# Kernel optimization log

Measured on AMD Instinct MI355X. Metric: run time of the kernel, lower is better.

Reference implementation:

```python
import jax, jax.numpy as jnp
import numpy as np

N_NODES = 100000
N_EDGES = 3200000


def setup_inputs() -> dict:
    key = jax.random.key(0)
    k = jax.random.split(key, 6)
    x = jax.random.normal(k[0], (N_NODES, 3), dtype=jnp.float32)
    edge_index = jax.random.randint(k[1], (2, N_EDGES), 0, N_NODES, dtype=jnp.int64)
    # Glorot-ish init for the two GCNConv layers (3->16, 16->7), bias=True (PyG default)
    W1 = jax.random.normal(k[2], (3, 16), dtype=jnp.float32) * (1.0 / np.sqrt(3.0))
    b1 = jnp.zeros((16,), dtype=jnp.float32)
    W2 = jax.random.normal(k[3], (16, 7), dtype=jnp.float32) * (1.0 / np.sqrt(16.0))
    b2 = jnp.zeros((7,), dtype=jnp.float32)
    return {"x": x, "edge_index": edge_index, "W1": W1, "b1": b1, "W2": W2, "b2": b2}


def _gcn_conv(x, W, b, src, dst, norm, n_nodes):
    # x: [N, Fin]; src/dst/norm: [E+N] (self-loops appended); out: [N, Fout]
    h = x @ W                                   # small GEMM
    msg = h[src] * norm[:, None]                # gather + scale per edge
    out = jax.ops.segment_sum(msg, dst, num_segments=n_nodes)  # scatter-add
    return out + b


def reference(x, edge_index, W1, b1, W2, b2):
    n = x.shape[0]
    loop = jnp.arange(n, dtype=edge_index.dtype)
    src = jnp.concatenate([edge_index[0], loop])
    dst = jnp.concatenate([edge_index[1], loop])
    # symmetric normalization D^-1/2 (A+I) D^-1/2, deg counted at targets
    deg = jax.ops.segment_sum(jnp.ones(src.shape[0], dtype=x.dtype), dst, num_segments=n)
    dinv = jnp.where(deg > 0, jax.lax.rsqrt(deg), 0.0)
    norm = dinv[src] * dinv[dst]                # [E+N]

    h = _gcn_conv(x, W1, b1, src, dst, norm, n)
    h = jax.nn.relu(h)
    h = _gcn_conv(h, W2, b2, src, dst, norm, n)
    return jax.nn.log_softmax(h, axis=1)
```

## Files before the change

kernel.cpp:

```cpp
#include <hip/hip_runtime.h>
#include <hip/hip_fp16.h>
#include <math.h>

#define N_NODES 100000
#define N_EDGES 3200000
#define NB 512
#define NPB 196
#define CAP 7168
#define EPB 12544
#define NBLK ((N_EDGES + EPB - 1) / EPB)

#define FSCALE 1048576.0f
#define INV_FSCALE (1.0f / 1048576.0f)


__device__ inline float2 h2f2(unsigned int u) {
    __half2 h = *reinterpret_cast<__half2*>(&u);
    return make_float2(__low2float(h), __high2float(h));
}

__device__ inline int fx(float v) { return __float2int_rn(v * FSCALE); }

__global__ void k_zero(int* __restrict__ gcur) {
    int i = blockIdx.x * blockDim.x + threadIdx.x;
    if (i < NB) gcur[i] = 0;
}

__global__ void __launch_bounds__(1024) k_bucket(
        const int* __restrict__ ei, int* __restrict__ gcur,
        unsigned int* __restrict__ bdata) {
    __shared__ int cnt[NB];
    __shared__ int gb[NB];
    int blk = blockIdx.x, tid = threadIdx.x;
    int e0 = blk * EPB;
    int ecnt = min(EPB, N_EDGES - e0);
    const int* dst = ei + N_EDGES + e0;
    const int* src = ei + e0;

    if (tid < NB) cnt[tid] = 0;
    __syncthreads();
    for (int i = tid; i < ecnt; i += 4096) {
        int i1 = i + 1024, i2 = i + 2048, i3 = i + 3072;
        int d0 = dst[i];
        int d1 = (i1 < ecnt) ? dst[i1] : 0;
        int d2 = (i2 < ecnt) ? dst[i2] : 0;
        int d3 = (i3 < ecnt) ? dst[i3] : 0;
        atomicAdd(&cnt[d0 / NPB], 1);
        if (i1 < ecnt) atomicAdd(&cnt[d1 / NPB], 1);
        if (i2 < ecnt) atomicAdd(&cnt[d2 / NPB], 1);
        if (i3 < ecnt) atomicAdd(&cnt[d3 / NPB], 1);
    }
    __syncthreads();
    if (tid < NB) {
        int c = cnt[tid];
        gb[tid] = (c > 0) ? atomicAdd(&gcur[tid], c) : 0;
        cnt[tid] = 0;
    }
    __syncthreads();
    for (int i = tid; i < ecnt; i += 4096) {
        int i1 = i + 1024, i2 = i + 2048, i3 = i + 3072;
        int d0 = dst[i];
        int s0 = src[i];
        int d1 = (i1 < ecnt) ? dst[i1] : 0;
        int s1 = (i1 < ecnt) ? src[i1] : 0;
        int d2 = (i2 < ecnt) ? dst[i2] : 0;
        int s2 = (i2 < ecnt) ? src[i2] : 0;
        int d3 = (i3 < ecnt) ? dst[i3] : 0;
        int s3 = (i3 < ecnt) ? src[i3] : 0;
        {
            int b = d0 / NPB, dl = d0 - b * NPB;
            int pos = atomicAdd(&cnt[b], 1) + gb[b];
            if (pos < CAP) bdata[(size_t)b * CAP + pos] = ((unsigned)dl << 17) | (unsigned)s0;
        }
        if (i1 < ecnt) {
            int b = d1 / NPB, dl = d1 - b * NPB;
            int pos = atomicAdd(&cnt[b], 1) + gb[b];
            if (pos < CAP) bdata[(size_t)b * CAP + pos] = ((unsigned)dl << 17) | (unsigned)s1;
        }
        if (i2 < ecnt) {
            int b = d2 / NPB, dl = d2 - b * NPB;
            int pos = atomicAdd(&cnt[b], 1) + gb[b];
            if (pos < CAP) bdata[(size_t)b * CAP + pos] = ((unsigned)dl << 17) | (unsigned)s2;
        }
        if (i3 < ecnt) {
            int b = d3 / NPB, dl = d3 - b * NPB;
            int pos = atomicAdd(&cnt[b], 1) + gb[b];
            if (pos < CAP) bdata[(size_t)b * CAP + pos] = ((unsigned)dl << 17) | (unsigned)s3;
        }
    }
}

__global__ void k_deg(const int* __restrict__ gcur, const unsigned int* __restrict__ bdata,
                      const float* __restrict__ x, __half2* __restrict__ xh) {
    __shared__ int cnt[NPB];
    int b = blockIdx.x, t = threadIdx.x;
    for (int j = t; j < NPB; j += 512) cnt[j] = 0;
    __syncthreads();
    int n = min(gcur[b], CAP);
    const unsigned int* p = bdata + (size_t)b * CAP;
    for (int e = t; e < n; e += 512) atomicAdd(&cnt[p[e] >> 17], 1);
    __syncthreads();
    int base = b * NPB;
    for (int j = t; j < NPB; j += 512) {
        int i = base + j;
        if (i < N_NODES) {
            float di = rsqrtf((float)cnt[j] + 1.0f);
            xh[2 * i + 0] = __floats2half2_rn(di * x[3 * i + 0], di * x[3 * i + 1]);
            xh[2 * i + 1] = __floats2half2_rn(di * x[3 * i + 2], di);
        }
    }
}

__global__ void __launch_bounds__(1024) k_l1(
        const int* __restrict__ gcur, const unsigned int* __restrict__ bdata,
        const __half2* __restrict__ xh, const float* __restrict__ W1,
        const float* __restrict__ b1, const float* __restrict__ W2,
        uint4* __restrict__ th) {
    __shared__ int a[NPB * 3];
    int b = blockIdx.x, tid = threadIdx.x;
    for (int j = tid; j < NPB * 3; j += 1024) a[j] = 0;
    __syncthreads();
    int n = min(gcur[b], CAP);
    const unsigned int* p = bdata + (size_t)b * CAP;
    const uint2* xg = (const uint2*)xh;
    for (int e = tid; e < n; e += 4096) {
        int e1 = e + 1024, e2 = e + 2048, e3 = e + 3072;
        unsigned int pk0 = p[e];
        unsigned int pk1 = (e1 < n) ? p[e1] : 0u;
        unsigned int pk2 = (e2 < n) ? p[e2] : 0u;
        unsigned int pk3 = (e3 < n) ? p[e3] : 0u;
        uint2 g0 = xg[pk0 & 0x1FFFF];
        uint2 g1 = (e1 < n) ? xg[pk1 & 0x1FFFF] : make_uint2(0u, 0u);
        uint2 g2 = (e2 < n) ? xg[pk2 & 0x1FFFF] : make_uint2(0u, 0u);
        uint2 g3 = (e3 < n) ? xg[pk3 & 0x1FFFF] : make_uint2(0u, 0u);
        {
            int dl = pk0 >> 17;
            float2 f01 = h2f2(g0.x), f2w = h2f2(g0.y);
            atomicAdd(&a[dl * 3 + 0], fx(f01.x));
            atomicAdd(&a[dl * 3 + 1], fx(f01.y));
            atomicAdd(&a[dl * 3 + 2], fx(f2w.x));
        }
        if (e1 < n) {
            int dl = pk1 >> 17;
            float2 f01 = h2f2(g1.x), f2w = h2f2(g1.y);
            atomicAdd(&a[dl * 3 + 0], fx(f01.x));
            atomicAdd(&a[dl * 3 + 1], fx(f01.y));
            atomicAdd(&a[dl * 3 + 2], fx(f2w.x));
        }
        if (e2 < n) {
            int dl = pk2 >> 17;
            float2 f01 = h2f2(g2.x), f2w = h2f2(g2.y);
            atomicAdd(&a[dl * 3 + 0], fx(f01.x));
            atomicAdd(&a[dl * 3 + 1], fx(f01.y));
            atomicAdd(&a[dl * 3 + 2], fx(f2w.x));
        }
        if (e3 < n) {
            int dl = pk3 >> 17;
            float2 f01 = h2f2(g3.x), f2w = h2f2(g3.y);
            atomicAdd(&a[dl * 3 + 0], fx(f01.x));
            atomicAdd(&a[dl * 3 + 1], fx(f01.y));
            atomicAdd(&a[dl * 3 + 2], fx(f2w.x));
        }
    }
    __syncthreads();
    int base = b * NPB;
    for (int j = tid; j < NPB; j += 1024) {
        int i = base + j;
        if (i >= N_NODES) continue;
        uint2 gi = xg[i];
        float2 f01 = h2f2(gi.x);
        float2 f2w = h2f2(gi.y);
        float di = f2w.y;
        float a0 = di * ((float)a[j * 3 + 0] * INV_FSCALE + f01.x);
        float a1 = di * ((float)a[j * 3 + 1] * INV_FSCALE + f01.y);
        float a2 = di * ((float)a[j * 3 + 2] * INV_FSCALE + f2w.x);
        float r[16];
#pragma unroll
        for (int k = 0; k < 16; ++k)
            r[k] = fmaxf(a0 * W1[k] + a1 * W1[16 + k] + a2 * W1[32 + k] + b1[k], 0.0f);
        float t[7];
#pragma unroll
        for (int c = 0; c < 7; ++c) {
            float v = 0.0f;
#pragma unroll
            for (int k = 0; k < 16; ++k) v += r[k] * W2[7 * k + c];
            t[c] = di * v;
        }
        __half2 h0 = __floats2half2_rn(t[0], t[1]);
        __half2 h1 = __floats2half2_rn(t[2], t[3]);
        __half2 h2 = __floats2half2_rn(t[4], t[5]);
        __half2 h3 = __floats2half2_rn(t[6], di);
        uint4 pk;
        pk.x = *reinterpret_cast<unsigned int*>(&h0);
        pk.y = *reinterpret_cast<unsigned int*>(&h1);
        pk.z = *reinterpret_cast<unsigned int*>(&h2);
        pk.w = *reinterpret_cast<unsigned int*>(&h3);
        th[i] = pk;
    }
}

__global__ void __launch_bounds__(1024) k_l2(
        const int* __restrict__ gcur, const unsigned int* __restrict__ bdata,
        const uint4* __restrict__ th, const float* __restrict__ b2,
        float* __restrict__ out) {
    __shared__ int a[NPB * 7];
    int b = blockIdx.x, tid = threadIdx.x;
    for (int j = tid; j < NPB * 7; j += 1024) a[j] = 0;
    __syncthreads();
    int n = min(gcur[b], CAP);
    const unsigned int* p = bdata + (size_t)b * CAP;
    for (int e = tid; e < n; e += 4096) {
        int e1 = e + 1024, e2 = e + 2048, e3 = e + 3072;
        unsigned int pk0 = p[e];
        unsigned int pk1 = (e1 < n) ? p[e1] : 0u;
        unsigned int pk2 = (e2 < n) ? p[e2] : 0u;
        unsigned int pk3 = (e3 < n) ? p[e3] : 0u;
        uint4 g0 = th[pk0 & 0x1FFFF];
        uint4 g1 = (e1 < n) ? th[pk1 & 0x1FFFF] : make_uint4(0u, 0u, 0u, 0u);
        uint4 g2 = (e2 < n) ? th[pk2 & 0x1FFFF] : make_uint4(0u, 0u, 0u, 0u);
        uint4 g3 = (e3 < n) ? th[pk3 & 0x1FFFF] : make_uint4(0u, 0u, 0u, 0u);
        {
            int dl = pk0 >> 17;
            float2 u0 = h2f2(g0.x), u1 = h2f2(g0.y), u2 = h2f2(g0.z), u3 = h2f2(g0.w);
            atomicAdd(&a[dl * 7 + 0], fx(u0.x));
            atomicAdd(&a[dl * 7 + 1], fx(u0.y));
            atomicAdd(&a[dl * 7 + 2], fx(u1.x));
            atomicAdd(&a[dl * 7 + 3], fx(u1.y));
            atomicAdd(&a[dl * 7 + 4], fx(u2.x));
            atomicAdd(&a[dl * 7 + 5], fx(u2.y));
            atomicAdd(&a[dl * 7 + 6], fx(u3.x));
        }
        if (e1 < n) {
            int dl = pk1 >> 17;
            float2 u0 = h2f2(g1.x), u1 = h2f2(g1.y), u2 = h2f2(g1.z), u3 = h2f2(g1.w);
            atomicAdd(&a[dl * 7 + 0], fx(u0.x));
            atomicAdd(&a[dl * 7 + 1], fx(u0.y));
            atomicAdd(&a[dl * 7 + 2], fx(u1.x));
            atomicAdd(&a[dl * 7 + 3], fx(u1.y));
            atomicAdd(&a[dl * 7 + 4], fx(u2.x));
            atomicAdd(&a[dl * 7 + 5], fx(u2.y));
            atomicAdd(&a[dl * 7 + 6], fx(u3.x));
        }
        if (e2 < n) {
            int dl = pk2 >> 17;
            float2 u0 = h2f2(g2.x), u1 = h2f2(g2.y), u2 = h2f2(g2.z), u3 = h2f2(g2.w);
            atomicAdd(&a[dl * 7 + 0], fx(u0.x));
            atomicAdd(&a[dl * 7 + 1], fx(u0.y));
            atomicAdd(&a[dl * 7 + 2], fx(u1.x));
            atomicAdd(&a[dl * 7 + 3], fx(u1.y));
            atomicAdd(&a[dl * 7 + 4], fx(u2.x));
            atomicAdd(&a[dl * 7 + 5], fx(u2.y));
            atomicAdd(&a[dl * 7 + 6], fx(u3.x));
        }
        if (e3 < n) {
            int dl = pk3 >> 17;
            float2 u0 = h2f2(g3.x), u1 = h2f2(g3.y), u2 = h2f2(g3.z), u3 = h2f2(g3.w);
            atomicAdd(&a[dl * 7 + 0], fx(u0.x));
            atomicAdd(&a[dl * 7 + 1], fx(u0.y));
            atomicAdd(&a[dl * 7 + 2], fx(u1.x));
            atomicAdd(&a[dl * 7 + 3], fx(u1.y));
            atomicAdd(&a[dl * 7 + 4], fx(u2.x));
            atomicAdd(&a[dl * 7 + 5], fx(u2.y));
            atomicAdd(&a[dl * 7 + 6], fx(u3.x));
        }
    }
    __syncthreads();
    int base = b * NPB;
    for (int j = tid; j < NPB; j += 1024) {
        int i = base + j;
        if (i >= N_NODES) continue;
        uint4 gi = th[i];
        float2 t0 = h2f2(gi.x), t1 = h2f2(gi.y), t2 = h2f2(gi.z), t3 = h2f2(gi.w);
        float di = t3.y;
        float thv[7] = {t0.x, t0.y, t1.x, t1.y, t2.x, t2.y, t3.x};
        float v[7];
        float m = -1e30f;
#pragma unroll
        for (int c = 0; c < 7; ++c) {
            v[c] = di * ((float)a[j * 7 + c] * INV_FSCALE + thv[c]) + b2[c];
            m = fmaxf(m, v[c]);
        }
        float sum = 0.0f;
#pragma unroll
        for (int c = 0; c < 7; ++c) sum += expf(v[c] - m);
        float lse = m + logf(sum);
#pragma unroll
        for (int c = 0; c < 7; ++c) out[7 * i + c] = v[c] - lse;
    }
}

extern "C" void kernel_launch(void* const* d_in, const int* in_sizes, int n_in,
                              void* d_out, int out_size, void* d_ws, size_t ws_size,
                              hipStream_t stream) {
    const float* x  = (const float*)d_in[0];
    const int*   ei = (const int*)d_in[1];
    const float* W1 = (const float*)d_in[2];
    const float* b1 = (const float*)d_in[3];
    const float* W2 = (const float*)d_in[4];
    const float* b2 = (const float*)d_in[5];
    float* out = (float*)d_out;

    char* ws = (char*)d_ws;
    int*          gcur  = (int*)ws;          ws += 4096;
    __half2*      xh    = (__half2*)ws;      ws += (size_t)N_NODES * 8;
    uint4*        th    = (uint4*)ws;        ws += (size_t)N_NODES * 16;
    unsigned int* bdata = (unsigned int*)ws;

    k_zero<<<2, 256, 0, stream>>>(gcur);
    k_bucket<<<NBLK, 1024, 0, stream>>>(ei, gcur, bdata);
    k_deg<<<NB, 512, 0, stream>>>(gcur, bdata, x, xh);
    k_l1<<<NB, 1024, 0, stream>>>(gcur, bdata, xh, W1, b1, W2, th);
    k_l2<<<NB, 1024, 0, stream>>>(gcur, bdata, th, b2, out);
}
```

Baseline: 77.07 us.

## Stage bucketed edges in LDS and write them out contiguously per bucket

The bucketing kernel first sorts each block's edges by bucket into shared memory, using a block-wide prefix scan over the bucket counts. It then writes them to global memory so that consecutive threads store to consecutive addresses within each bucket's run. This replaces scattered 4-byte global writes with mostly coalesced ones. The cost is about 50KB of LDS per block, a 9-step scan with barriers, and a binary search per element.

```diff
diff --git a/kernel.cpp b/kernel.cpp
--- a/kernel.cpp
+++ b/kernel.cpp
@@ -29,8 +29,11 @@
 __global__ void __launch_bounds__(1024) k_bucket(
         const int* __restrict__ ei, int* __restrict__ gcur,
         unsigned int* __restrict__ bdata) {
+    __shared__ unsigned int lds_pay[EPB];
     __shared__ int cnt[NB];
     __shared__ int gb[NB];
+    __shared__ int sc[NB];
+    __shared__ int psum[NB + 1];
     int blk = blockIdx.x, tid = threadIdx.x;
     int e0 = blk * EPB;
     int ecnt = min(EPB, N_EDGES - e0);
@@ -54,6 +57,19 @@
     if (tid < NB) {
         int c = cnt[tid];
         gb[tid] = (c > 0) ? atomicAdd(&gcur[tid], c) : 0;
+        sc[tid] = c;
+    }
+    __syncthreads();
+    for (int off = 1; off < NB; off <<= 1) {
+        int v = 0;
+        if (tid < NB && tid >= off) v = sc[tid - off];
+        __syncthreads();
+        if (tid < NB) sc[tid] += v;
+        __syncthreads();
+    }
+    if (tid < NB) {
+        psum[tid + 1] = sc[tid];
+        if (tid == 0) psum[0] = 0;
         cnt[tid] = 0;
     }
     __syncthreads();
@@ -69,24 +85,34 @@
         int s3 = (i3 < ecnt) ? src[i3] : 0;
         {
             int b = d0 / NPB, dl = d0 - b * NPB;
-            int pos = atomicAdd(&cnt[b], 1) + gb[b];
-            if (pos < CAP) bdata[(size_t)b * CAP + pos] = ((unsigned)dl << 17) | (unsigned)s0;
+            int lp = atomicAdd(&cnt[b], 1) + psum[b];
+            lds_pay[lp] = ((unsigned)dl << 17) | (unsigned)s0;
         }
         if (i1 < ecnt) {
             int b = d1 / NPB, dl = d1 - b * NPB;
-            int pos = atomicAdd(&cnt[b], 1) + gb[b];
-            if (pos < CAP) bdata[(size_t)b * CAP + pos] = ((unsigned)dl << 17) | (unsigned)s1;
+            int lp = atomicAdd(&cnt[b], 1) + psum[b];
+            lds_pay[lp] = ((unsigned)dl << 17) | (unsigned)s1;
         }
         if (i2 < ecnt) {
             int b = d2 / NPB, dl = d2 - b * NPB;
-            int pos = atomicAdd(&cnt[b], 1) + gb[b];
-            if (pos < CAP) bdata[(size_t)b * CAP + pos] = ((unsigned)dl << 17) | (unsigned)s2;
+            int lp = atomicAdd(&cnt[b], 1) + psum[b];
+            lds_pay[lp] = ((unsigned)dl << 17) | (unsigned)s2;
         }
         if (i3 < ecnt) {
             int b = d3 / NPB, dl = d3 - b * NPB;
-            int pos = atomicAdd(&cnt[b], 1) + gb[b];
-            if (pos < CAP) bdata[(size_t)b * CAP + pos] = ((unsigned)dl << 17) | (unsigned)s3;
-        }
+            int lp = atomicAdd(&cnt[b], 1) + psum[b];
+            lds_pay[lp] = ((unsigned)dl << 17) | (unsigned)s3;
+        }
+    }
+    __syncthreads();
+    for (int e = tid; e < ecnt; e += 1024) {
+        int lo = 0, hi = NB;
+        while (hi - lo > 1) {
+            int mid = (lo + hi) >> 1;
+            if (psum[mid] <= e) lo = mid; else hi = mid;
+        }
+        int gp = gb[lo] + (e - psum[lo]);
+        if (gp < CAP) bdata[(size_t)lo * CAP + gp] = lds_pay[e];
     }
 }
 
```

New measurement: 74.47 us. -3.4%, faster.
